# Kernel tuning notes

Hardware: AMD Instinct MI355X
Metric: run time of the kernel (lower is better)

## Reference

```python
import jax, jax.numpy as jnp
import numpy as np

B, F, PER_FIELD_VOCAB, K = 32768, 16, 65536, 8
FEATURE_LEN = F * PER_FIELD_VOCAB


def setup_inputs() -> dict:
    key = jax.random.key(0)
    k1, k2, k3 = jax.random.split(key, 3)
    inputs = jax.random.randint(k1, (B, F), 0, PER_FIELD_VOCAB)  # raw per-field ids
    w0 = jnp.zeros((1,), dtype=jnp.float32)
    w = jax.random.normal(k2, (FEATURE_LEN, 1), dtype=jnp.float32) * 0.05
    v = jax.random.normal(k3, (FEATURE_LEN, F, K), dtype=jnp.float32) * 0.05
    return {"inputs": inputs, "w0": w0, "w": w, "v": v}


def reference(inputs, w0, w, v):
    # index_mapping: add per-field offset so each field indexes its own vocab slice
    Fn = v.shape[1]
    per_field = w.shape[0] // Fn
    idx = inputs + jnp.arange(Fn, dtype=inputs.dtype) * per_field  # [B, F]

    # first order: w0 + sum over fields of gathered linear weights -> [B, 1]
    first_order = w0 + jnp.sum(w[idx], axis=1)

    # latent_vector = sum over the gather's field axis: [B, F, F, K] -> [B, F, K]
    lv = jnp.sum(v[idx], axis=1)

    # sum_{i<j} <lv_i, lv_j> = 0.5 * ((sum_i lv_i)^2 - sum_i lv_i^2), reduced over K
    s = jnp.sum(lv, axis=1)                         # [B, K]
    sq = jnp.sum(lv * lv, axis=1)                   # [B, K]
    second_order = 0.5 * jnp.sum(s * s - sq, axis=1, keepdims=True)  # [B, 1]

    return first_order + second_order
```

## Files before the change

kernel.cpp:

```cpp
#include <hip/hip_runtime.h>


constexpr int F   = 16;
constexpr int K   = 8;
constexpr int PFV = 65536;
constexpr int ROW = F * K;

__global__ __launch_bounds__(256) void ffm_fwd(
    const int* __restrict__ idx, const float* __restrict__ w0,
    const float* __restrict__ w, const float* __restrict__ v,
    float* __restrict__ out, int nB)
{
  const int gtid = blockIdx.x * 256 + threadIdx.x;
  const int b    = gtid >> 6;
  const int lane = threadIdx.x & 63;
  if (b >= nB) return;

  int   my   = 0;
  float wsum = 0.f;
  if (lane < F) {
    my   = idx[b * F + lane] + lane * PFV;
    wsum = w[my];
  }

  const int half = lane >> 5;
  const int c    = lane & 31;

  float4 acc = make_float4(0.f, 0.f, 0.f, 0.f);
#pragma unroll
  for (int t = 0; t < F / 2; ++t) {
    const int r = __shfl(my, 2 * t + half, 64);
    const float4* row = (const float4*)(v + (size_t)r * ROW);
    const float4 x = row[c];
    acc.x += x.x; acc.y += x.y; acc.z += x.z; acc.w += x.w;
  }

  acc.x += __shfl_xor(acc.x, 32, 64);
  acc.y += __shfl_xor(acc.y, 32, 64);
  acc.z += __shfl_xor(acc.z, 32, 64);
  acc.w += __shfl_xor(acc.w, 32, 64);

  float q = acc.x * acc.x + acc.y * acc.y + acc.z * acc.z + acc.w * acc.w;

  float4 s = acc;
#pragma unroll
  for (int m = 2; m <= 16; m <<= 1) {
    s.x += __shfl_xor(s.x, m, 64);
    s.y += __shfl_xor(s.y, m, 64);
    s.z += __shfl_xor(s.z, m, 64);
    s.w += __shfl_xor(s.w, m, 64);
  }
  float sp = s.x * s.x + s.y * s.y + s.z * s.z + s.w * s.w;
  sp += __shfl_xor(sp, 1, 64);

#pragma unroll
  for (int m = 1; m <= 16; m <<= 1) {
    q    += __shfl_xor(q, m, 64);
    wsum += __shfl_xor(wsum, m, 64);
  }

  if (lane == 0)
    out[b] = w0[0] + wsum + 0.5f * (sp - q);
}

extern "C" void kernel_launch(void* const* d_in, const int* in_sizes, int n_in,
                              void* d_out, int out_size, void* d_ws, size_t ws_size,
                              hipStream_t stream) {
  const int*   idx = (const int*)d_in[0];
  const float* w0  = (const float*)d_in[1];
  const float* w   = (const float*)d_in[2];
  const float* v   = (const float*)d_in[3];
  float*       out = (float*)d_out;

  const int nB = in_sizes[0] / F;
  const int blocks = (nB + 3) / 4;
  ffm_fwd<<<blocks, 256, 0, stream>>>(idx, w0, w, v, out, nB);
}
```

Measured before the change: 50.77 us.

## Process two batch rows per wavefront, one per half-wave

Each 64-lane wavefront now handles two samples, with each 32-lane half gathering all 16 rows for its own sample. The cross-half reduction goes away, and the grid is half the size. The aim is to cut per-sample index loads and shuffle overhead and to improve lane utilisation on the w/idx loads. In exchange each lane issues twice as many serial gather loads, which lowers memory-level parallelism per wave.

New measurement: 51.73 us. Within noise of the previous version (+1.9%).

```diff
diff --git a/kernel.cpp b/kernel.cpp
--- a/kernel.cpp
+++ b/kernel.cpp
@@ -2,43 +2,36 @@
 
 
 constexpr int F   = 16;
-constexpr int K   = 8;
 constexpr int PFV = 65536;
-constexpr int ROW = F * K;
+constexpr int ROW = 128;
 
-__global__ __launch_bounds__(256) void ffm_fwd(
+__global__ __launch_bounds__(256) void ffm_fwd2(
     const int* __restrict__ idx, const float* __restrict__ w0,
     const float* __restrict__ w, const float* __restrict__ v,
     float* __restrict__ out, int nB)
 {
-  const int gtid = blockIdx.x * 256 + threadIdx.x;
-  const int b    = gtid >> 6;
+  const int wid  = (blockIdx.x * 256 + threadIdx.x) >> 6;
   const int lane = threadIdx.x & 63;
-  if (b >= nB) return;
-
-  int   my   = 0;
-  float wsum = 0.f;
-  if (lane < F) {
-    my   = idx[b * F + lane] + lane * PFV;
-    wsum = w[my];
-  }
-
   const int half = lane >> 5;
   const int c    = lane & 31;
 
+  const int b0 = wid * 2;
+  int bs = b0 + half;
+  if (b0 >= nB) return;
+  if (bs >= nB) bs = nB - 1;
+
+  const int f  = c & 15;
+  const int my = idx[bs * F + f] + f * PFV;
+  const float wv = w[my];
+
   float4 acc = make_float4(0.f, 0.f, 0.f, 0.f);
 #pragma unroll
-  for (int t = 0; t < F / 2; ++t) {
-    const int r = __shfl(my, 2 * t + half, 64);
+  for (int t = 0; t < F; ++t) {
+    const int r = __shfl(my, t + (half << 5), 64);
     const float4* row = (const float4*)(v + (size_t)r * ROW);
     const float4 x = row[c];
     acc.x += x.x; acc.y += x.y; acc.z += x.z; acc.w += x.w;
   }
-
-  acc.x += __shfl_xor(acc.x, 32, 64);
-  acc.y += __shfl_xor(acc.y, 32, 64);
-  acc.z += __shfl_xor(acc.z, 32, 64);
-  acc.w += __shfl_xor(acc.w, 32, 64);
 
   float q = acc.x * acc.x + acc.y * acc.y + acc.z * acc.z + acc.w * acc.w;
 
@@ -53,14 +46,16 @@
   float sp = s.x * s.x + s.y * s.y + s.z * s.z + s.w * s.w;
   sp += __shfl_xor(sp, 1, 64);
 
+  float wsum = wv;
 #pragma unroll
-  for (int m = 1; m <= 16; m <<= 1) {
+  for (int m = 1; m <= 8; m <<= 1) {
     q    += __shfl_xor(q, m, 64);
     wsum += __shfl_xor(wsum, m, 64);
   }
+  q += __shfl_xor(q, 16, 64);
 
-  if (lane == 0)
-    out[b] = w0[0] + wsum + 0.5f * (sp - q);
+  if (c == 0 && b0 + half < nB)
+    out[b0 + half] = w0[0] + wsum + 0.5f * (sp - q);
 }
 
 extern "C" void kernel_launch(void* const* d_in, const int* in_sizes, int n_in,
@@ -73,6 +68,7 @@
   float*       out = (float*)d_out;
 
   const int nB = in_sizes[0] / F;
-  const int blocks = (nB + 3) / 4;
-  ffm_fwd<<<blocks, 256, 0, stream>>>(idx, w0, w, v, out, nB);
+  const int nWaves  = (nB + 1) / 2;
+  const int blocks  = (nWaves + 3) / 4;
+  ffm_fwd2<<<blocks, 256, 0, stream>>>(idx, w0, w, v, out, nB);
 }
```
